# Performance work log

Hardware: AMD Instinct MI355X
Metric: run time of the kernel (lower is better)

## Reference

```python
import jax, jax.numpy as jnp
import numpy as np

# CDF 9/7 (JPEG2000 irreversible) analysis filters
H0 = np.array([0.026748757410810, -0.016864118442875, -0.078223266528990,
               0.266864118442875, 0.602949018236360, 0.266864118442875,
               -0.078223266528990, -0.016864118442875, 0.026748757410810], np.float32)
H1 = np.array([0.091271763114250, -0.057543526228500, -0.591271763114250,
               1.115087052457000, -0.591271763114250, -0.057543526228500,
               0.091271763114250], np.float32)


def conv2d(x, w, stride=(1, 1), padding='VALID', groups=1):
    return jax.lax.conv_general_dilated(
        x, w, stride, padding,
        dimension_numbers=('NCHW', 'OIHW', 'NCHW'),
        feature_group_count=groups)


def partial_spectral_conv(x, mask, weight, bias, u):
    # spectral normalization (one power iteration with fixed u buffer)
    O = weight.shape[0]
    wm = weight.reshape(O, -1)
    v = wm.T @ u
    v = v / (jnp.linalg.norm(v) + 1e-12)
    sigma = jnp.linalg.norm(wm @ v)
    w_sn = weight / sigma
    # partial convolution (NVIDIA-style mask renormalization)
    kh, kw = weight.shape[2], weight.shape[3]
    out = conv2d(x * mask, w_sn, padding=((1, 1), (1, 1)))           # [B,O,H,W]
    msum = conv2d(mask, jnp.ones((1, 1, kh, kw), x.dtype), padding=((1, 1), (1, 1)))
    valid = msum > 0
    ratio = jnp.where(valid, (kh * kw) / jnp.maximum(msum, 1e-8), 0.0)
    out = jnp.where(valid, out * ratio + bias[None, :, None, None], 0.0)
    return out, valid.astype(x.dtype)                                # mask stays [B,1,H,W]


def partial_gdn(x, mask, beta, gamma):
    # divisive normalization: y = x / sqrt(beta + gamma @ x^2), masked
    denom = jnp.sqrt(beta[None, :, None, None] + jnp.einsum('oc,bchw->bohw', gamma, x * x))
    return (x / denom) * mask, mask


def filt(x, f, axis):
    # grouped 1D filter along H (axis=2) or W (axis=3), reflect pad, stride 2
    K = f.shape[0]
    p = (K - 1) // 2
    pads = [(0, 0)] * 4
    pads[axis] = (p, p)
    xp = jnp.pad(x, pads, mode='reflect')
    C = x.shape[1]
    if axis == 2:
        kern = jnp.broadcast_to(f.reshape(1, 1, K, 1), (C, 1, K, 1))
        stride = (2, 1)
    else:
        kern = jnp.broadcast_to(f.reshape(1, 1, 1, K), (C, 1, 1, K))
        stride = (1, 2)
    return conv2d(xp, kern, stride, 'VALID', groups=C)


def mask_down(m, K, axis):
    # mask is valid where any contributing pixel is valid
    cnt = filt(m, jnp.ones((K,), m.dtype), axis)
    return (cnt > 0).astype(m.dtype)


def dwt2d(x, mask):
    h0 = jnp.asarray(H0)
    h1 = jnp.asarray(H1)
    lo_r, hi_r = filt(x, h0, 2), filt(x, h1, 2)
    ll, lh = filt(lo_r, h0, 3), filt(lo_r, h1, 3)
    hl, hh = filt(hi_r, h0, 3), filt(hi_r, h1, 3)
    m_lo, m_hi = mask_down(mask, 9, 2), mask_down(mask, 7, 2)
    m_ll, m_lh = mask_down(m_lo, 9, 3), mask_down(m_lo, 7, 3)
    m_hl, m_hh = mask_down(m_hi, 9, 3), mask_down(m_hi, 7, 3)
    return (ll, lh, hl, hh), (m_ll, m_lh, m_hl, m_hh)


def setup_inputs() -> dict:
    key = jax.random.key(0)
    ks = jax.random.split(key, 6)
    B, Cin, Cout, H, W = 8, 64, 128, 256, 256
    tensor = jax.random.normal(ks[0], (B, Cin, H, W), jnp.float32)
    mask = (jax.random.uniform(ks[1], (B, 1, H, W)) > 0.2).astype(jnp.float32)
    weight = jax.random.normal(ks[2], (Cout, Cin, 3, 3), jnp.float32) * 0.05
    bias = jnp.zeros((Cout,), jnp.float32)
    u = jax.random.normal(ks[3], (Cout,), jnp.float32)
    u = u / jnp.linalg.norm(u)
    beta = jnp.ones((Cout,), jnp.float32)
    gamma = 0.1 * jnp.eye(Cout, dtype=jnp.float32) + 1e-3
    return {"tensor": tensor, "mask": mask, "weight": weight, "bias": bias,
            "u": u, "beta": beta, "gamma": gamma}


def reference(tensor, mask, weight, bias, u, beta, gamma):
    x, m = partial_spectral_conv(tensor, mask, weight, bias, u)
    x, m = partial_gdn(x, m, beta, gamma)
    (ll, lh, hl, hh), (m_ll, m_lh, m_hl, m_hh) = dwt2d(x, m)
    return (ll, m_ll, lh, hl, hh, m_lh, m_hl, m_hh)
```

## Files before the change

kernel.cpp:

```cpp
#include <hip/hip_runtime.h>

#define B 8
#define CIN 64
#define COUT 128
#define H 256
#define W 256
#define HW 65536
#define OH 128
#define OW 128

typedef __attribute__((ext_vector_type(8))) short bf16x8;
typedef __attribute__((ext_vector_type(16))) float f32x16;
typedef __attribute__((ext_vector_type(4))) float f32x4;
typedef __attribute__((ext_vector_type(2))) float f32x2;

__constant__ float c_h0[9] = {0.026748757410810f, -0.016864118442875f, -0.078223266528990f,
                              0.266864118442875f, 0.602949018236360f, 0.266864118442875f,
                              -0.078223266528990f, -0.016864118442875f, 0.026748757410810f};
__constant__ float c_h1[7] = {0.091271763114250f, -0.057543526228500f, -0.591271763114250f,
                              1.115087052457000f, -0.591271763114250f, -0.057543526228500f,
                              0.091271763114250f};

__device__ __forceinline__ unsigned short f2bf(float f) {
    unsigned int x = __float_as_uint(f);
    unsigned int r = (x + 0x7fffu + ((x >> 16) & 1u)) >> 16;
    return (unsigned short)r;
}
__device__ __forceinline__ float bf2f(unsigned short h) {
    return __uint_as_float(((unsigned int)h) << 16);
}
__device__ __forceinline__ int refl(int i) {
    if (i < 0) return -i;
    if (i > 255) return 510 - i;
    return i;
}

__global__ void sigma_kernel(const float* __restrict__ w, const float* __restrict__ u,
                             float* __restrict__ inv_sigma) {
    __shared__ float v[576];
    __shared__ float red[1024];
    __shared__ float d2[128];
    const int tid = threadIdx.x;
    if (tid < 576) {
        float s = 0.f;
        for (int o = 0; o < 128; ++o) s += w[o * 576 + tid] * u[o];
        v[tid] = s;
    }
    __syncthreads();
    red[tid] = (tid < 576) ? v[tid] * v[tid] : 0.f;
    __syncthreads();
    for (int off = 512; off > 0; off >>= 1) {
        if (tid < off) red[tid] += red[tid + off];
        __syncthreads();
    }
    const float vn = sqrtf(red[0]) + 1e-12f;
    __syncthreads();
    const int o = tid >> 3, p = tid & 7;
    const float* wr = w + o * 576 + p * 72;
    const float* vv = v + p * 72;
    float part = 0.f;
    for (int j = 0; j < 72; j += 4) {
        const f32x4 wv = *(const f32x4*)(wr + j);
        part += wv.x * vv[j] + wv.y * vv[j + 1] + wv.z * vv[j + 2] + wv.w * vv[j + 3];
    }
    red[tid] = part;
    __syncthreads();
    if (tid < 128) {
        float d = 0.f;
        for (int k = 0; k < 8; ++k) d += red[tid * 8 + k];
        d /= vn;
        d2[tid] = d * d;
    }
    __syncthreads();
    for (int off = 64; off > 0; off >>= 1) {
        if (tid < off) d2[tid] += d2[tid + off];
        __syncthreads();
    }
    if (tid == 0) inv_sigma[0] = 1.f / sqrtf(d2[0]);
}

__global__ void prep_kernel(const float* __restrict__ w, const float* __restrict__ gamma,
                            const float* __restrict__ inv_sigma,
                            unsigned short* __restrict__ wt_bf,
                            unsigned short* __restrict__ gamma_bf) {
    const int i = blockIdx.x * 256 + threadIdx.x;
    const float is = inv_sigma[0];
    if (i < 73728) {
        const int o = i / 576, rem = i - o * 576;
        const int c = rem / 9, tap = rem - c * 9;
        wt_bf[(o * 9 + tap) * 64 + c] = f2bf(w[i] * is);
    } else if (i < 90112) {
        const int j = i - 73728;
        gamma_bf[j] = f2bf(gamma[j]);
    }
}

__global__ __launch_bounds__(256, 3) void convgdn_kernel(
    const float* __restrict__ x, const float* __restrict__ mask,
    const unsigned short* __restrict__ wt_bf, const float* __restrict__ bias,
    const unsigned short* __restrict__ gamma_bf, const float* __restrict__ beta,
    unsigned short* __restrict__ t, float* __restrict__ valid) {
    __shared__ __align__(16) char lds[38192];
    unsigned short* raw = (unsigned short*)lds;
    unsigned short* y2  = (unsigned short*)lds;
    float* mlds = (float*)(lds + 36864);
    float* rlds = (float*)(lds + 37680);

    const int tid = threadIdx.x;
    const int lane = tid & 63;
    const int lo = lane & 31;
    const int hi = lane >> 5;
    const int n0 = (tid >> 6) << 5;
    const int oc = n0 + lo;
    const int bid = blockIdx.x;
    const int work = ((bid & 7) << 9) | (bid >> 3);
    const int b = work >> 9;
    const int rem0 = work & 511;
    const int h0 = (rem0 >> 3) << 2;
    const int wc0 = (rem0 & 7) << 5;

    if (tid < 204) {
        const int r = tid / 34, cl = tid - r * 34;
        const int hr = h0 - 1 + r, wc = wc0 - 1 + cl;
        float mv = 0.f;
        if (hr >= 0 && hr < H && wc >= 0 && wc < W) mv = mask[b * HW + hr * W + wc];
        mlds[tid] = mv;
    }
    __syncthreads();

    const bool intr = (h0 != 0) && (h0 != 252) && (wc0 != 0) && (wc0 != 224);
    if (intr) {
        const float* xb = x + ((size_t)b * CIN) * HW + (h0 - 1) * W + (wc0 - 4);
        for (unsigned i = tid; i < 1920u; i += 256u) {
            const unsigned q = i % 10u;
            const unsigned rc = i / 10u;
            const unsigned r = rc % 6u;
            const unsigned cp = rc / 6u;
            const float* p0 = xb + (2u * cp) * HW + r * W + 4u * q;
            const f32x4 va = *(const f32x4*)p0;
            const f32x4 vb2 = *(const f32x4*)(p0 + HW);
            unsigned short* base = &raw[((r * 8u + (cp >> 2)) * 34u) * 8u + 2u * (cp & 3u)];
            const float* mrow = &mlds[r * 34u];
#pragma unroll
            for (int k = 0; k < 4; ++k) {
                const int cl = 4 * (int)q - 3 + k;
                if ((unsigned)cl <= 33u) {
                    const float mv = mrow[cl];
                    const unsigned int pk = (unsigned int)f2bf(va[k] * mv) |
                                            ((unsigned int)f2bf(vb2[k] * mv) << 16);
                    *(unsigned int*)(base + (unsigned)cl * 8u) = pk;
                }
            }
        }
    } else {
        for (unsigned i = tid; i < 13056u; i += 256u) {
            const unsigned c = i / 204u, rem = i - c * 204u;
            const unsigned r = rem / 34u, cl = rem - r * 34u;
            const int hr = h0 - 1 + (int)r, wc = wc0 - 1 + (int)cl;
            float v = 0.f;
            if (hr >= 0 && hr < H && wc >= 0 && wc < W)
                v = x[((b * CIN + (int)c) * H + hr) * W + wc] * mlds[rem];
            raw[((r * 8u + (c >> 3)) * 34u + cl) * 8u + (c & 7u)] = f2bf(v);
        }
    }
    if (tid < 128) {
        const int mt = tid >> 5, cl = tid & 31;
        float ms = 0.f;
#pragma unroll
        for (int a = 0; a < 3; ++a)
#pragma unroll
            for (int bb = 0; bb < 3; ++bb) ms += mlds[(mt + a) * 34 + cl + bb];
        const bool vld = ms > 0.f;
        rlds[tid] = vld ? 9.f / fmaxf(ms, 1e-8f) : 0.f;
        valid[b * HW + (h0 + mt) * W + wc0 + cl] = vld ? 1.f : 0.f;
    }
    __syncthreads();

    f32x16 acc[4];
#pragma unroll
    for (int mt = 0; mt < 4; ++mt)
#pragma unroll
        for (int r = 0; r < 16; ++r) acc[mt][r] = 0.f;

    for (int kh = 0; kh < 3; ++kh) {
#pragma unroll
        for (int kw = 0; kw < 3; ++kw) {
            const int tap = kh * 3 + kw;
            bf16x8 bw[4];
#pragma unroll
            for (int cc = 0; cc < 4; ++cc)
                bw[cc] = *(const bf16x8*)&wt_bf[(oc * 9 + tap) * 64 + cc * 16 + hi * 8];
#pragma unroll
            for (int cc = 0; cc < 4; ++cc) {
                const int c0 = cc * 16 + hi * 8;
#pragma unroll
                for (int mt = 0; mt < 4; ++mt) {
                    const bf16x8 afrag =
                        *(const bf16x8*)&raw[(((mt + kh) * 8 + (c0 >> 3)) * 34 + (lo + kw)) * 8];
                    acc[mt] = __builtin_amdgcn_mfma_f32_32x32x16_bf16(afrag, bw[cc], acc[mt], 0, 0, 0);
                }
            }
        }
    }
    __syncthreads();

    const float bs = bias[oc];
    const float bt = beta[oc];
#pragma unroll
    for (int mt = 0; mt < 4; ++mt) {
#pragma unroll
        for (int r = 0; r < 16; ++r) {
            const int rowq = (r & 3) + 8 * (r >> 2) + 4 * hi;
            const float rat = rlds[mt * 32 + rowq];
            const float y = (rat > 0.f) ? acc[mt][r] * rat + bs : 0.f;
            acc[mt][r] = y;
            y2[(mt * 32 + rowq) * 144 + (oc ^ ((rowq & 7) << 3))] = f2bf(y * y);
        }
    }
    __syncthreads();

#pragma unroll
    for (int mt = 0; mt < 4; ++mt) {
        f32x16 a2;
#pragma unroll
        for (int r = 0; r < 16; ++r) a2[r] = 0.f;
        const int row = mt * 32 + lo;
        const int swz = (lo & 7) << 3;
#pragma unroll
        for (int ch = 0; ch < 8; ++ch) {
            const int c0 = ch * 16 + hi * 8;
            const bf16x8 gb = *(const bf16x8*)&gamma_bf[oc * 128 + c0];
            const bf16x8 ga = *(const bf16x8*)&y2[row * 144 + (c0 ^ swz)];
            a2 = __builtin_amdgcn_mfma_f32_32x32x16_bf16(ga, gb, a2, 0, 0, 0);
        }
        __syncthreads();
        unsigned short* yg = (unsigned short*)lds + mt * 4608;
#pragma unroll
        for (int rg = 0; rg < 4; ++rg) {
            ushort4 pk;
            unsigned short* pp = (unsigned short*)&pk;
#pragma unroll
            for (int j = 0; j < 4; ++j) {
                const int r = rg * 4 + j;
                const float d = bt + a2[r];
                pp[j] = f2bf(acc[mt][r] * rsqrtf(d));
            }
            const int pxc = 2 * rg + hi;
            *(ushort4*)&yg[oc * 36 + ((pxc ^ (oc & 7)) << 2)] = pk;
        }
    }
    __syncthreads();

#pragma unroll
    for (int it = 0; it < 2; ++it) {
        const int idx = it * 256 + tid;
        const int oc2 = idx & 127, mt2 = idx >> 7;
        const unsigned short* src = (const unsigned short*)lds + mt2 * 4608 + oc2 * 36;
        unsigned short* dst = &t[((b * COUT + oc2) * H + h0 + mt2) * W + wc0];
        const int s7 = oc2 & 7;
#pragma unroll
        for (int k = 0; k < 8; ++k)
            *(ushort4*)(dst + k * 4) = *(const ushort4*)(src + ((k ^ s7) << 2));
    }
}

__global__ void dwt_kernel(const unsigned short* __restrict__ y, float* __restrict__ out) {
    __shared__ float ys[40][76];
    __shared__ float lof[16][76];
    __shared__ float hif[16][76];
    const int tid = threadIdx.x;
    const int bid = blockIdx.x;
    const int work = ((bid & 7) << 12) | (bid >> 3);
    const int bc = work >> 5;
    const int tile = work & 31;
    const int wt_ = tile & 3;
    const int ht_ = tile >> 2;
    const int ho0 = ht_ * 16, wo0 = wt_ * 32;
    const int r0 = 2 * ho0 - 4, c0 = 2 * wo0 - 4;
    const unsigned short* yb = y + bc * HW;

    ushort4 va[3];
    int ldst[3];
#pragma unroll
    for (int k = 0; k < 3; ++k) {
        const int i = tid + (k << 8);
        ldst[k] = -1;
        if (i < 720) {
            const int lr = i / 18;
            const int ch4 = (i - lr * 18) << 2;
            const int col = c0 + ch4;
            if ((unsigned)col <= 252u) {
                va[k] = *(const ushort4*)(yb + refl(r0 + lr) * W + col);
                ldst[k] = lr * 76 + ch4;
            }
        }
    }
#pragma unroll
    for (int k = 0; k < 3; ++k) {
        if (ldst[k] >= 0) {
            f32x4 f;
            f.x = bf2f(va[k].x); f.y = bf2f(va[k].y); f.z = bf2f(va[k].z); f.w = bf2f(va[k].w);
            *(f32x4*)&((float*)ys)[ldst[k]] = f;
        }
    }
    if (wt_ == 0) {
        for (int i = tid; i < 160; i += 256) {
            const int lr = i >> 2, q = i & 3;
            ys[lr][q] = bf2f(yb[refl(r0 + lr) * W + (4 - q)]);
        }
    } else if (wt_ == 3) {
        for (int i = tid; i < 160; i += 256) {
            const int lr = i >> 2, q = i & 3;
            ys[lr][68 + q] = bf2f(yb[refl(r0 + lr) * W + (254 - q)]);
        }
    }
    __syncthreads();

    for (unsigned i = tid; i < 288u; i += 256u) {
        const int r = (int)(i / 18u);
        const int ch4 = (int)(i - (unsigned)r * 18u) << 2;
        f32x4 vv[9];
#pragma unroll
        for (int k = 0; k < 9; ++k) vv[k] = *(const f32x4*)&ys[2 * r + k][ch4];
        f32x4 sl = c_h0[0] * vv[0];
#pragma unroll
        for (int k = 1; k < 9; ++k) sl += c_h0[k] * vv[k];
        f32x4 sh = c_h1[0] * vv[1];
#pragma unroll
        for (int k = 1; k < 7; ++k) sh += c_h1[k] * vv[k + 1];
        *(f32x4*)&lof[r][ch4] = sl;
        *(f32x4*)&hif[r][ch4] = sh;
    }
    __syncthreads();

    const int rr = tid >> 4;
    const int q = tid & 15;
    const f32x4 a0 = *(const f32x4*)&lof[rr][4 * q];
    const f32x4 a1 = *(const f32x4*)&lof[rr][4 * q + 4];
    const f32x4 a2 = *(const f32x4*)&lof[rr][4 * q + 8];
    const f32x4 b0 = *(const f32x4*)&hif[rr][4 * q];
    const f32x4 b1 = *(const f32x4*)&hif[rr][4 * q + 4];
    const f32x4 b2 = *(const f32x4*)&hif[rr][4 * q + 8];
    float L[12], M[12];
#pragma unroll
    for (int m = 0; m < 4; ++m) {
        L[m] = a0[m]; L[m + 4] = a1[m]; L[m + 8] = a2[m];
        M[m] = b0[m]; M[m + 4] = b1[m]; M[m + 8] = b2[m];
    }
    float ll0 = 0.f, ll1 = 0.f, hl0 = 0.f, hl1 = 0.f;
#pragma unroll
    for (int k = 0; k < 9; ++k) {
        ll0 += c_h0[k] * L[k];
        ll1 += c_h0[k] * L[k + 2];
        hl0 += c_h0[k] * M[k];
        hl1 += c_h0[k] * M[k + 2];
    }
    float lh0 = 0.f, lh1 = 0.f, hh0 = 0.f, hh1 = 0.f;
#pragma unroll
    for (int k = 0; k < 7; ++k) {
        lh0 += c_h1[k] * L[k + 1];
        lh1 += c_h1[k] * L[k + 3];
        hh0 += c_h1[k] * M[k + 1];
        hh1 += c_h1[k] * M[k + 3];
    }
    const int idx = (bc * OH + ho0 + rr) * OW + wo0 + 2 * q;
    f32x2 s;
    s.x = ll0; s.y = ll1; *(f32x2*)&out[idx] = s;
    s.x = lh0; s.y = lh1; *(f32x2*)&out[16908288 + idx] = s;
    s.x = hl0; s.y = hl1; *(f32x2*)&out[33685504 + idx] = s;
    s.x = hh0; s.y = hh1; *(f32x2*)&out[50462720 + idx] = s;
}

__global__ void dwtmask_kernel(const float* __restrict__ valid, float* __restrict__ out) {
    const int g = blockIdx.x * 256 + threadIdx.x;
    const int b = g >> 14;
    const int rem = g & 16383;
    const int i = rem >> 7, j = rem & 127;
    const float* vb = valid + b * HW;
    bool bll = false, blh = false, bhl = false, bhh = false;
    for (int k1 = 0; k1 < 9; ++k1) {
        const int rr = refl(2 * i - 4 + k1);
        const bool in7r = (k1 >= 1 && k1 <= 7);
        for (int k2 = 0; k2 < 9; ++k2) {
            const int cc = refl(2 * j - 4 + k2);
            if (vb[rr * W + cc] > 0.f) {
                const bool in7c = (k2 >= 1 && k2 <= 7);
                bll = true;
                blh |= in7c;
                bhl |= in7r;
                bhh |= (in7r && in7c);
            }
        }
    }
    out[16777216 + g] = bll ? 1.f : 0.f;
    out[67239936 + g] = blh ? 1.f : 0.f;
    out[67371008 + g] = bhl ? 1.f : 0.f;
    out[67502080 + g] = bhh ? 1.f : 0.f;
}

extern "C" void kernel_launch(void* const* d_in, const int* in_sizes, int n_in,
                              void* d_out, int out_size, void* d_ws, size_t ws_size,
                              hipStream_t stream) {
    const float* x     = (const float*)d_in[0];
    const float* mask  = (const float*)d_in[1];
    const float* w     = (const float*)d_in[2];
    const float* bias  = (const float*)d_in[3];
    const float* u     = (const float*)d_in[4];
    const float* beta  = (const float*)d_in[5];
    const float* gamma = (const float*)d_in[6];
    float* out = (float*)d_out;

    float* f_ws = (float*)d_ws;
    float* inv_sigma = f_ws;
    unsigned short* wt_bf    = (unsigned short*)(f_ws + 256);
    unsigned short* gamma_bf = wt_bf + 73728;
    float* valid = (float*)(gamma_bf + 16384);
    unsigned short* t = (unsigned short*)(valid + 524288);

    sigma_kernel<<<1, 1024, 0, stream>>>(w, u, inv_sigma);
    prep_kernel<<<352, 256, 0, stream>>>(w, gamma, inv_sigma, wt_bf, gamma_bf);
    convgdn_kernel<<<4096, 256, 0, stream>>>(x, mask, wt_bf, bias, gamma_bf, beta, t, valid);
    dwt_kernel<<<32768, 256, 0, stream>>>(t, out);
    dwtmask_kernel<<<512, 256, 0, stream>>>(valid, out);
}
```

Baseline: 673.5 us.

## Raise convgdn occupancy, restage output per row, drop a DWT barrier

The conv+GDN kernel raises its launch-bounds occupancy hint from 3 to 4 and reorganises LDS to match. The mask is stored as bf16, the y² buffer loses its XOR swizzle and uses a tighter stride, and the output staging gets its own region, written and flushed per row-half with 16-byte stores. The interior input load now packs 8 channels per thread straight into the raw layout. The DWT kernel assigns filter rows per warp so a block barrier becomes a wavefront-local wait, and the sigma kernel caches u in LDS. Dropping the swizzle and using more barriers in the store loop may add LDS bank conflicts and sync overhead, and a fourth block per CU is not guaranteed by register use.

```diff
diff --git a/kernel.cpp b/kernel.cpp
--- a/kernel.cpp
+++ b/kernel.cpp
@@ -40,10 +40,14 @@
     __shared__ float v[576];
     __shared__ float red[1024];
     __shared__ float d2[128];
+    __shared__ float us[128];
     const int tid = threadIdx.x;
+    if (tid < 128) us[tid] = u[tid];
+    __syncthreads();
     if (tid < 576) {
         float s = 0.f;
-        for (int o = 0; o < 128; ++o) s += w[o * 576 + tid] * u[o];
+#pragma unroll 4
+        for (int o = 0; o < 128; ++o) s += w[o * 576 + tid] * us[o];
         v[tid] = s;
     }
     __syncthreads();
@@ -95,16 +99,17 @@
     }
 }
 
-__global__ __launch_bounds__(256, 3) void convgdn_kernel(
+__global__ __launch_bounds__(256, 4) void convgdn_kernel(
     const float* __restrict__ x, const float* __restrict__ mask,
     const unsigned short* __restrict__ wt_bf, const float* __restrict__ bias,
     const unsigned short* __restrict__ gamma_bf, const float* __restrict__ beta,
     unsigned short* __restrict__ t, float* __restrict__ valid) {
-    __shared__ __align__(16) char lds[38192];
+    __shared__ __align__(16) char lds[40864];
     unsigned short* raw = (unsigned short*)lds;
     unsigned short* y2  = (unsigned short*)lds;
-    float* mlds = (float*)(lds + 36864);
-    float* rlds = (float*)(lds + 37680);
+    unsigned short* yg  = (unsigned short*)(lds + 34816);
+    unsigned short* mlds16 = (unsigned short*)(lds + 39936);
+    float* rlds = (float*)(lds + 40352);
 
     const int tid = threadIdx.x;
     const int lane = tid & 63;
@@ -124,33 +129,26 @@
         const int hr = h0 - 1 + r, wc = wc0 - 1 + cl;
         float mv = 0.f;
         if (hr >= 0 && hr < H && wc >= 0 && wc < W) mv = mask[b * HW + hr * W + wc];
-        mlds[tid] = mv;
+        mlds16[tid] = f2bf(mv);
     }
     __syncthreads();
 
     const bool intr = (h0 != 0) && (h0 != 252) && (wc0 != 0) && (wc0 != 224);
     if (intr) {
-        const float* xb = x + ((size_t)b * CIN) * HW + (h0 - 1) * W + (wc0 - 4);
-        for (unsigned i = tid; i < 1920u; i += 256u) {
-            const unsigned q = i % 10u;
-            const unsigned rc = i / 10u;
-            const unsigned r = rc % 6u;
-            const unsigned cp = rc / 6u;
-            const float* p0 = xb + (2u * cp) * HW + r * W + 4u * q;
-            const f32x4 va = *(const f32x4*)p0;
-            const f32x4 vb2 = *(const f32x4*)(p0 + HW);
-            unsigned short* base = &raw[((r * 8u + (cp >> 2)) * 34u) * 8u + 2u * (cp & 3u)];
-            const float* mrow = &mlds[r * 34u];
-#pragma unroll
-            for (int k = 0; k < 4; ++k) {
-                const int cl = 4 * (int)q - 3 + k;
-                if ((unsigned)cl <= 33u) {
-                    const float mv = mrow[cl];
-                    const unsigned int pk = (unsigned int)f2bf(va[k] * mv) |
-                                            ((unsigned int)f2bf(vb2[k] * mv) << 16);
-                    *(unsigned int*)(base + (unsigned)cl * 8u) = pk;
-                }
-            }
+        for (unsigned i = tid; i < 1632u; i += 256u) {
+            const unsigned cl = i % 34u;
+            const unsigned ro = i / 34u;
+            const unsigned oct = ro & 7u;
+            const unsigned r = ro >> 3u;
+            const float m = bf2f(mlds16[r * 34u + cl]);
+            const float* px = x + ((size_t)(b * CIN + (int)(oct * 8u))) * HW +
+                              (h0 - 1 + (int)r) * W + (wc0 - 1 + (int)cl);
+            uint4 pk;
+            pk.x = (unsigned)f2bf(px[0] * m)      | ((unsigned)f2bf(px[HW] * m) << 16);
+            pk.y = (unsigned)f2bf(px[2 * HW] * m) | ((unsigned)f2bf(px[3 * HW] * m) << 16);
+            pk.z = (unsigned)f2bf(px[4 * HW] * m) | ((unsigned)f2bf(px[5 * HW] * m) << 16);
+            pk.w = (unsigned)f2bf(px[6 * HW] * m) | ((unsigned)f2bf(px[7 * HW] * m) << 16);
+            *(uint4*)&raw[i * 8u] = pk;
         }
     } else {
         for (unsigned i = tid; i < 13056u; i += 256u) {
@@ -159,7 +157,7 @@
             const int hr = h0 - 1 + (int)r, wc = wc0 - 1 + (int)cl;
             float v = 0.f;
             if (hr >= 0 && hr < H && wc >= 0 && wc < W)
-                v = x[((b * CIN + (int)c) * H + hr) * W + wc] * mlds[rem];
+                v = x[((b * CIN + (int)c) * H + hr) * W + wc] * bf2f(mlds16[rem]);
             raw[((r * 8u + (c >> 3)) * 34u + cl) * 8u + (c & 7u)] = f2bf(v);
         }
     }
@@ -169,7 +167,7 @@
 #pragma unroll
         for (int a = 0; a < 3; ++a)
 #pragma unroll
-            for (int bb = 0; bb < 3; ++bb) ms += mlds[(mt + a) * 34 + cl + bb];
+            for (int bb = 0; bb < 3; ++bb) ms += bf2f(mlds16[(mt + a) * 34 + cl + bb]);
         const bool vld = ms > 0.f;
         rlds[tid] = vld ? 9.f / fmaxf(ms, 1e-8f) : 0.f;
         valid[b * HW + (h0 + mt) * W + wc0 + cl] = vld ? 1.f : 0.f;
@@ -214,7 +212,7 @@
             const float rat = rlds[mt * 32 + rowq];
             const float y = (rat > 0.f) ? acc[mt][r] * rat + bs : 0.f;
             acc[mt][r] = y;
-            y2[(mt * 32 + rowq) * 144 + (oc ^ ((rowq & 7) << 3))] = f2bf(y * y);
+            y2[(mt * 32 + rowq) * 136 + oc] = f2bf(y * y);
         }
     }
     __syncthreads();
@@ -225,42 +223,43 @@
 #pragma unroll
         for (int r = 0; r < 16; ++r) a2[r] = 0.f;
         const int row = mt * 32 + lo;
-        const int swz = (lo & 7) << 3;
 #pragma unroll
         for (int ch = 0; ch < 8; ++ch) {
             const int c0 = ch * 16 + hi * 8;
             const bf16x8 gb = *(const bf16x8*)&gamma_bf[oc * 128 + c0];
-            const bf16x8 ga = *(const bf16x8*)&y2[row * 144 + (c0 ^ swz)];
+            const bf16x8 ga = *(const bf16x8*)&y2[row * 136 + c0];
             a2 = __builtin_amdgcn_mfma_f32_32x32x16_bf16(ga, gb, a2, 0, 0, 0);
         }
-        __syncthreads();
-        unsigned short* yg = (unsigned short*)lds + mt * 4608;
-#pragma unroll
-        for (int rg = 0; rg < 4; ++rg) {
-            ushort4 pk;
-            unsigned short* pp = (unsigned short*)&pk;
-#pragma unroll
-            for (int j = 0; j < 4; ++j) {
-                const int r = rg * 4 + j;
-                const float d = bt + a2[r];
-                pp[j] = f2bf(acc[mt][r] * rsqrtf(d));
+#pragma unroll
+        for (int half = 0; half < 2; ++half) {
+#pragma unroll
+            for (int rg2 = 0; rg2 < 2; ++rg2) {
+                const int rg = 2 * half + rg2;
+                ushort4 pk;
+                unsigned short* pp = (unsigned short*)&pk;
+#pragma unroll
+                for (int j = 0; j < 4; ++j) {
+                    const int r = rg * 4 + j;
+                    const float d = bt + a2[r];
+                    pp[j] = f2bf(acc[mt][r] * rsqrtf(d));
+                }
+                const int lp = 2 * rg2 + hi;
+                *(ushort4*)&yg[oc * 20 + lp * 4] = pk;
             }
-            const int pxc = 2 * rg + hi;
-            *(ushort4*)&yg[oc * 36 + ((pxc ^ (oc & 7)) << 2)] = pk;
-        }
-    }
-    __syncthreads();
-
-#pragma unroll
-    for (int it = 0; it < 2; ++it) {
-        const int idx = it * 256 + tid;
-        const int oc2 = idx & 127, mt2 = idx >> 7;
-        const unsigned short* src = (const unsigned short*)lds + mt2 * 4608 + oc2 * 36;
-        unsigned short* dst = &t[((b * COUT + oc2) * H + h0 + mt2) * W + wc0];
-        const int s7 = oc2 & 7;
-#pragma unroll
-        for (int k = 0; k < 8; ++k)
-            *(ushort4*)(dst + k * 4) = *(const ushort4*)(src + ((k ^ s7) << 2));
+            __syncthreads();
+            {
+                const int oc2 = tid >> 1, seg = tid & 1;
+                const unsigned short* src = &yg[oc2 * 20 + seg * 8];
+                const uint2 p0 = *(const uint2*)src;
+                const uint2 p1 = *(const uint2*)(src + 4);
+                uint4 sv;
+                sv.x = p0.x; sv.y = p0.y; sv.z = p1.x; sv.w = p1.y;
+                unsigned short* dst =
+                    &t[((b * COUT + oc2) * H + h0 + mt) * W + wc0 + half * 16 + seg * 8];
+                *(uint4*)dst = sv;
+            }
+            __syncthreads();
+        }
     }
 }
 
@@ -316,9 +315,12 @@
     }
     __syncthreads();
 
-    for (unsigned i = tid; i < 288u; i += 256u) {
-        const int r = (int)(i / 18u);
-        const int ch4 = (int)(i - (unsigned)r * 18u) << 2;
+    const int warp = tid >> 6, ln = tid & 63;
+    {
+        const int it = ln;
+        const int rr_ = it / 18;
+        const int r = warp * 4 + rr_;
+        const int ch4 = (it - rr_ * 18) << 2;
         f32x4 vv[9];
 #pragma unroll
         for (int k = 0; k < 9; ++k) vv[k] = *(const f32x4*)&ys[2 * r + k][ch4];
@@ -331,7 +333,23 @@
         *(f32x4*)&lof[r][ch4] = sl;
         *(f32x4*)&hif[r][ch4] = sh;
     }
-    __syncthreads();
+    if (ln < 8) {
+        const int r = warp * 4 + 3;
+        const int ch4 = (10 + ln) << 2;
+        f32x4 vv[9];
+#pragma unroll
+        for (int k = 0; k < 9; ++k) vv[k] = *(const f32x4*)&ys[2 * r + k][ch4];
+        f32x4 sl = c_h0[0] * vv[0];
+#pragma unroll
+        for (int k = 1; k < 9; ++k) sl += c_h0[k] * vv[k];
+        f32x4 sh = c_h1[0] * vv[1];
+#pragma unroll
+        for (int k = 1; k < 7; ++k) sh += c_h1[k] * vv[k + 1];
+        *(f32x4*)&lof[r][ch4] = sl;
+        *(f32x4*)&hif[r][ch4] = sh;
+    }
+    asm volatile("s_waitcnt lgkmcnt(0)" ::: "memory");
+    __builtin_amdgcn_sched_barrier(0);
 
     const int rr = tid >> 4;
     const int q = tid & 15;
```

Result: no change. 674.4 us (+0.1%).
